# Optimization experiments

Measured on AMD Instinct MI355X. Metric: run time of the kernel, lower is better.

Reference implementation:

```python
import jax, jax.numpy as jnp
import numpy as np

NEG_INF = -jnp.inf


def setup_inputs() -> dict:
    B, V = 128, 128000
    key = jax.random.key(0)
    k1, k2, k3, k4, k5 = jax.random.split(key, 5)
    logits = jax.random.normal(k1, (B, V), dtype=jnp.float32)
    # temperatures in [0.1, 1.0) to avoid divide-by-tiny blowups
    temperatures = jax.random.uniform(k2, (B,), dtype=jnp.float32) * 0.9 + 0.1
    # min_p typically small, in [0, 0.1)
    min_ps = jax.random.uniform(k3, (B,), dtype=jnp.float32) * 0.1
    # top_p in [0.1, 1.0)
    top_ps = jax.random.uniform(k4, (B,), dtype=jnp.float32) * 0.9 + 0.1
    # top_k in [1, 1000)
    top_ks = jax.random.randint(k5, (B,), 1, 1000, dtype=jnp.int32)
    return {"logits": logits, "temperatures": temperatures, "min_ps": min_ps,
            "top_ps": top_ps, "top_ks": top_ks}


def _apply_top_k_top_p(logits, top_ps, top_ks):
    B, V = logits.shape
    sort_idx = jnp.argsort(logits, axis=-1)  # ascending, matches torch sort(descending=False)
    logits_sort = jnp.take_along_axis(logits, sort_idx, axis=-1)
    # top-k: threshold is the (V-k)-th smallest value; mask anything strictly below it
    thresh_idx = (V - top_ks.astype(jnp.int32))[:, None]          # [B,1]
    thresh = jnp.take_along_axis(logits_sort, thresh_idx, axis=-1)  # [B,1]
    logits_sort = jnp.where(logits_sort < thresh, NEG_INF, logits_sort)
    # top-p: drop smallest tokens whose cumulative prob <= 1 - p; never drop the max token
    probs_sort = jax.nn.softmax(logits_sort, axis=-1)
    probs_sum = jnp.cumsum(probs_sort, axis=-1)
    top_p_mask = probs_sum <= (1.0 - top_ps)[:, None]
    top_p_mask = top_p_mask.at[:, -1].set(False)
    logits_sort = jnp.where(top_p_mask, NEG_INF, logits_sort)
    # scatter back to original vocab order
    rows = jnp.arange(B)[:, None]
    return jnp.zeros_like(logits_sort).at[rows, sort_idx].set(logits_sort)


def _apply_min_p(logits, min_ps):
    probs = jax.nn.softmax(logits, axis=-1)
    top_probs = jnp.max(probs, axis=-1, keepdims=True)
    remove = probs < min_ps[:, None] * top_probs
    return jnp.where(remove, NEG_INF, logits)


def reference(logits, temperatures, min_ps, top_ps, top_ks):
    logits = logits.astype(jnp.float32) / temperatures[:, None]
    logits = _apply_top_k_top_p(logits, top_ps, top_ks)
    logits = _apply_min_p(logits, min_ps)
    # torch.multinomial(softmax(logits), 1) == categorical sampling from logits
    sample_key = jax.random.key(42)
    next_tokens = jax.random.categorical(sample_key, logits, axis=-1)  # [B]
    return next_tokens
```

## Files before the change

kernel.cpp:

```cpp
#include <hip/hip_runtime.h>
#include <stdint.h>

#define HBINS 4096
#define CAND 4096
#define SCAP 2048
#define CSLICES 16
#define CTHREADS 256
#define STHREADS 1024
#define TLOC 128
#define STAGECAP 1024

typedef unsigned int u32;
typedef unsigned long long u64;

__device__ __forceinline__ u32 f2s(float f) {
  u32 b = __float_as_uint(f);
  return b ^ ((b & 0x80000000u) ? 0xFFFFFFFFu : 0x80000000u);
}
__device__ __forceinline__ float s2f(u32 s) {
  u32 b = (s & 0x80000000u) ? (s ^ 0x80000000u) : ~s;
  return __uint_as_float(b);
}
__device__ __forceinline__ u32 rotl32(u32 x, int r) { return (x << r) | (x >> (32 - r)); }

__device__ __forceinline__ u64 shfl_xor_u64(u64 v, int mask) {
  int lo = __shfl_xor((int)(u32)v, mask, 64);
  int hi = __shfl_xor((int)(u32)(v >> 32), mask, 64);
  return ((u64)(u32)hi << 32) | (u32)lo;
}

__device__ __forceinline__ u32 threefry_bits(u32 ctr) {
  const u32 ks0 = 0u, ks1 = 42u, ks2 = 0x1BD11BDAu ^ 0u ^ 42u;
  u32 x0 = ks0;
  u32 x1 = ctr + ks1;
#define TFR(r) { x0 += x1; x1 = rotl32(x1, (r)); x1 ^= x0; }
  TFR(13) TFR(15) TFR(26) TFR(6)   x0 += ks1; x1 += ks2 + 1u;
  TFR(17) TFR(29) TFR(16) TFR(24)  x0 += ks2; x1 += ks0 + 2u;
  TFR(13) TFR(15) TFR(26) TFR(6)   x0 += ks0; x1 += ks1 + 3u;
  TFR(17) TFR(29) TFR(16) TFR(24)  x0 += ks1; x1 += ks2 + 4u;
  TFR(13) TFR(15) TFR(26) TFR(6)   x0 += ks2; x1 += ks0 + 5u;
#undef TFR
  return x0 ^ x1;
}

__global__ __launch_bounds__(CTHREADS)
void collect2_kernel(const float* __restrict__ logits,
                     const float* __restrict__ temps,
                     u32* __restrict__ gcount,
                     u64* __restrict__ gcand, int V, int slice_len) {
  const int row = blockIdx.x / CSLICES;
  const int sl  = blockIdx.x % CSLICES;
  const int tid = threadIdx.x;

  __shared__ u32 hist[HBINS];
  __shared__ u64 stage[STAGECAP];
  __shared__ u32 part[CTHREADS];
  __shared__ u32 chunkv[64];
  __shared__ int sh_thr, sh_cnt, sh_base;

  for (int i = tid; i < HBINS; i += CTHREADS) hist[i] = 0u;
  __syncthreads();

  int rem = V - sl * slice_len;
  if (rem > slice_len) rem = slice_len;
  if (rem < 0) rem = 0;
  const float* src = logits + (size_t)row * (size_t)V + (size_t)sl * slice_len;
  const int n4 = rem >> 2;
  const float4* p4 = (const float4*)src;

  for (int i = tid; i < n4; i += CTHREADS) {
    float4 w = p4[i];
    atomicAdd(&hist[f2s(w.x) >> 20], 1u);
    atomicAdd(&hist[f2s(w.y) >> 20], 1u);
    atomicAdd(&hist[f2s(w.z) >> 20], 1u);
    atomicAdd(&hist[f2s(w.w) >> 20], 1u);
  }
  for (int i = (n4 << 2) + tid; i < rem; i += CTHREADS)
    atomicAdd(&hist[f2s(src[i]) >> 20], 1u);
  __syncthreads();

  {
    u32 s = 0;
    for (int j = 0; j < 16; ++j) s += hist[tid * 16 + j];
    part[tid] = s;
  }
  __syncthreads();
  if (tid < 64)
    chunkv[tid] = part[tid * 4] + part[tid * 4 + 1] + part[tid * 4 + 2] + part[tid * 4 + 3];
  __syncthreads();
  if (tid == 0) {
    u32 ku = (u32)((rem < TLOC) ? (rem > 0 ? rem : 1) : TLOC);
    u32 acc = 0;
    int cstar = 0;
    for (int c = 63; c >= 0; --c) {
      if (acc + chunkv[c] >= ku) { cstar = c; break; }
      acc += chunkv[c];
    }
    int pstar = cstar * 4;
    for (int p = cstar * 4 + 3; p >= cstar * 4; --p) {
      if (acc + part[p] >= ku) { pstar = p; break; }
      acc += part[p];
    }
    int bstar = pstar * 16;
    for (int bq = pstar * 16 + 15; bq >= pstar * 16; --bq) {
      acc += hist[bq];
      if (acc >= ku) { bstar = bq; break; }
    }
    sh_thr = (int)(((u32)bstar) << 20);
    sh_cnt = 0;
  }
  __syncthreads();

  const u32 thr = (u32)sh_thr;
  const float t = temps[row];
  const u32 ibase = (u32)(sl * slice_len);
  for (int i = tid; i < n4; i += CTHREADS) {
    float4 w = p4[i];
    if (f2s(w.x) >= thr) { int pos = atomicAdd(&sh_cnt, 1); if (pos < STAGECAP) stage[pos] = ((u64)f2s(w.x / t) << 32) | (ibase + 4u * i + 0u); }
    if (f2s(w.y) >= thr) { int pos = atomicAdd(&sh_cnt, 1); if (pos < STAGECAP) stage[pos] = ((u64)f2s(w.y / t) << 32) | (ibase + 4u * i + 1u); }
    if (f2s(w.z) >= thr) { int pos = atomicAdd(&sh_cnt, 1); if (pos < STAGECAP) stage[pos] = ((u64)f2s(w.z / t) << 32) | (ibase + 4u * i + 2u); }
    if (f2s(w.w) >= thr) { int pos = atomicAdd(&sh_cnt, 1); if (pos < STAGECAP) stage[pos] = ((u64)f2s(w.w / t) << 32) | (ibase + 4u * i + 3u); }
  }
  for (int i = (n4 << 2) + tid; i < rem; i += CTHREADS) {
    float lg = src[i];
    if (f2s(lg) >= thr) { int pos = atomicAdd(&sh_cnt, 1); if (pos < STAGECAP) stage[pos] = ((u64)f2s(lg / t) << 32) | (ibase + (u32)i); }
  }
  __syncthreads();
  int n = sh_cnt;
  if (n > STAGECAP) n = STAGECAP;
  if (tid == 0) sh_base = (int)atomicAdd(&gcount[row], (u32)n);
  __syncthreads();
  const int base = sh_base;
  u64* gc = gcand + (size_t)row * CAND;
  for (int i = tid; i < n; i += CTHREADS) {
    int dst = base + i;
    if (dst < CAND) gc[dst] = stage[i];
  }
}

__global__ __launch_bounds__(STHREADS)
void Sampler_73529840107542_kernel(const float* __restrict__ minps,
                                   const float* __restrict__ topps,
                                   const int* __restrict__ topks,
                                   const u32* __restrict__ gcount,
                                   const u64* __restrict__ gcand,
                                   int* __restrict__ out, int V) {
  const int b = blockIdx.x;
  const int tid = threadIdx.x;
  const int w = tid >> 6, l = tid & 63;
  const float one_minus_p = 1.0f - topps[b];
  const float minp = minps[b];
  int k = topks[b];
  if (k < 1) k = 1;
  if (k > V) k = V;

  __shared__ __align__(16) unsigned char arena[50176];
  u64* cand   = (u64*)(arena);
  float* eBuf = (float*)(arena);
  unsigned char* keepf = arena + 8192;
  u64* scand  = (u64*)(arena + 32768);
  u32* rbin   = (u32*)(arena + 49152);
  __shared__ float wredf[16];
  __shared__ u64 wred64[16];
  __shared__ int sh_byte, sh_above, sh_ns;
  __shared__ float sh_Z1, sh_Z2;

  int cs = (int)gcount[b];
  if (cs > CAND) cs = CAND;
  const u64* gc = gcand + (size_t)b * CAND;
  for (int c = tid; c < cs; c += STHREADS) cand[c] = gc[c];
  if (tid == 0) sh_ns = 0;
  __syncthreads();

  u32 prefix = 0u;
  u32 remk = (u32)k;
  for (int pass = 0; pass < 4; ++pass) {
    const int shift = 24 - 8 * pass;
    if (tid < 256) rbin[tid] = 0u;
    __syncthreads();
    const u32 mask = (pass == 0) ? 0u : (0xFFFFFFFFu << (shift + 8));
    const int iters = (cs + STHREADS - 1) / STHREADS;
    for (int it = 0; it < iters; ++it) {
      int c = it * STHREADS + tid;
      bool active = false;
      u32 bin = 0;
      if (c < cs) {
        u32 s = (u32)(cand[c] >> 32);
        if (((s ^ prefix) & mask) == 0u) { active = true; bin = (s >> shift) & 255u; }
      }
      u64 ball = __ballot(active);
      while (ball) {
        int leader = __ffsll((unsigned long long)ball) - 1;
        u32 lbin = (u32)__shfl((int)bin, leader, 64);
        u64 same = __ballot(active && bin == lbin);
        if (l == leader) atomicAdd(&rbin[lbin], (u32)__popcll(same));
        ball &= ~same;
      }
    }
    __syncthreads();
    if (w == 0) {
      u32 b0 = rbin[4 * l], b1 = rbin[4 * l + 1], b2 = rbin[4 * l + 2], b3 = rbin[4 * l + 3];
      u32 q3 = b3, q2 = b2 + q3, q1 = b1 + q2, q0 = b0 + q1;
      u32 inc = q0;
#pragma unroll
      for (int off = 1; off < 64; off <<= 1) {
        int src = l + off;
        u32 o = (u32)__shfl((int)inc, src < 64 ? src : l, 64);
        inc += (src < 64) ? o : 0u;
      }
      u32 excl = inc - q0;
      u64 ball = __ballot(excl + q0 >= remk);
      int lsel = 63 - __clzll(ball);
      if (l == lsel) {
        int i; u32 above;
        if      (excl + q3 >= remk) { i = 3; above = excl; }
        else if (excl + q2 >= remk) { i = 2; above = excl + q3; }
        else if (excl + q1 >= remk) { i = 1; above = excl + q2; }
        else                        { i = 0; above = excl + q1; }
        sh_byte = 4 * l + i;
        sh_above = (int)above;
      }
    }
    __syncthreads();
    prefix |= ((u32)sh_byte) << shift;
    remk -= (u32)sh_above;
  }
  const u32 Ts = prefix;

  for (int c = tid; c < cs; c += STHREADS) {
    u64 key = cand[c];
    if ((u32)(key >> 32) >= Ts) {
      int pos = atomicAdd(&sh_ns, 1);
      if (pos < SCAP) scand[pos] = key;
    }
  }
  __syncthreads();
  int ns = sh_ns;
  if (ns > SCAP) ns = SCAP;

  int SN = 128;
  while (SN < ns) SN <<= 1;
  const int NW = SN >> 7;
  const bool act = (w < NW);
  const int e_lo = (w << 7) + l;
  const int e_hi = e_lo + 64;
  const u64 SENT = 0xFFFFFFFFFFFFFFFFull;
  u64 k0 = (act && e_lo < ns) ? scand[e_lo] : SENT;
  u64 k1 = (act && e_hi < ns) ? scand[e_hi] : SENT;
  for (int size = 2; size <= SN; size <<= 1) {
    for (int s = size >> 1; s > 0; s >>= 1) {
      if (s >= 128) {
        if (act) { scand[e_lo] = k0; scand[e_hi] = k1; }
        __syncthreads();
        if (act) {
          u64 p0 = scand[e_lo ^ s], p1 = scand[e_hi ^ s];
          bool km0 = (((e_lo & s) == 0) == ((e_lo & size) == 0));
          if (km0 ? (p0 < k0) : (p0 > k0)) k0 = p0;
          bool km1 = (((e_hi & s) == 0) == ((e_hi & size) == 0));
          if (km1 ? (p1 < k1) : (p1 > k1)) k1 = p1;
        }
        __syncthreads();
      } else if (act) {
        if (s == 64) {
          bool asc = ((e_lo & size) == 0);
          if ((k0 > k1) == asc) { u64 t = k0; k0 = k1; k1 = t; }
        } else {
          u64 p0 = shfl_xor_u64(k0, s);
          u64 p1 = shfl_xor_u64(k1, s);
          bool km0 = (((l & s) == 0) == ((e_lo & size) == 0));
          if (km0 ? (p0 < k0) : (p0 > k0)) k0 = p0;
          bool km1 = (((l & s) == 0) == ((e_hi & size) == 0));
          if (km1 ? (p1 < k1) : (p1 > k1)) k1 = p1;
        }
      }
    }
  }
  if (act) { scand[e_lo] = k0; scand[e_hi] = k1; }
  __syncthreads();

  const float m = s2f((u32)(scand[ns - 1] >> 32));

  for (int c = tid; c < ns; c += STHREADS)
    eBuf[c] = expf(s2f((u32)(scand[c] >> 32)) - m);
  __syncthreads();

  {
    float local = 0.0f;
    for (int c = tid; c < ns; c += STHREADS) local += eBuf[c];
#pragma unroll
    for (int off = 1; off < 64; off <<= 1) local += __shfl_xor(local, off, 64);
    if (l == 0) wredf[w] = local;
    __syncthreads();
    if (w == 0) {
      float v = (l < 16) ? wredf[l] : 0.0f;
#pragma unroll
      for (int off = 1; off < 64; off <<= 1) v += __shfl_xor(v, off, 64);
      if (l == 0) sh_Z1 = v;
    }
    __syncthreads();
  }
  const float Z1 = sh_Z1;

  if (w == 0) {
    float carry = 0.0f;
    for (int base2 = 0; base2 < ns; base2 += 64) {
      int c = base2 + l;
      float v = (c < ns) ? (eBuf[c] / Z1) : 0.0f;
      float acc = carry;
#pragma unroll 16
      for (int j = 0; j < 64; ++j) {
        float t = __shfl(v, j, 64);
        acc += (l >= j) ? t : 0.0f;
      }
      if (c < ns)
        keepf[c] = (c == ns - 1 || acc > one_minus_p) ? 1 : 0;
      carry = __shfl(acc, 63, 64);
    }
  }
  __syncthreads();

  {
    float local = 0.0f;
    for (int c = tid; c < ns; c += STHREADS)
      if (keepf[c]) local += eBuf[c];
#pragma unroll
    for (int off = 1; off < 64; off <<= 1) local += __shfl_xor(local, off, 64);
    if (l == 0) wredf[w] = local;
    __syncthreads();
    if (w == 0) {
      float v = (l < 16) ? wredf[l] : 0.0f;
#pragma unroll
      for (int off = 1; off < 64; off <<= 1) v += __shfl_xor(v, off, 64);
      if (l == 0) sh_Z2 = v;
    }
    __syncthreads();
  }

  {
    const float Z2 = sh_Z2;
    const float rhs = minp * (1.0f / Z2);
    for (int c = tid; c < ns; c += STHREADS)
      if (keepf[c] && (eBuf[c] / Z2 < rhs)) keepf[c] = 0;
  }
  __syncthreads();

  {
    const float TINY = 1.17549435082228750797e-38f;
    u64 best = 0ull;
    for (int c = tid; c < ns; c += STHREADS) {
      if (!keepf[c]) continue;
      u32 s = (u32)(scand[c] >> 32);
      u32 idx = (u32)(scand[c] & 0xFFFFFFFFull);
      float x = s2f(s);
      u32 bits = threefry_bits((u32)b * (u32)V + idx);
      float f = __uint_as_float((bits >> 9) | 0x3f800000u) - 1.0f;
      float u = fmaxf(TINY, f * 1.0f + TINY);
      float g = -logf(-logf(u));
      float sc = g + x;
      u64 key = ((u64)f2s(sc) << 32) | (u64)(0xFFFFFFFFu - idx);
      if (key > best) best = key;
    }
#pragma unroll
    for (int off = 1; off < 64; off <<= 1) {
      u64 o = shfl_xor_u64(best, off);
      if (o > best) best = o;
    }
    if (l == 0) wred64[w] = best;
    __syncthreads();
    if (w == 0) {
      u64 v = (l < 16) ? wred64[l] : 0ull;
#pragma unroll
      for (int off = 1; off < 64; off <<= 1) {
        u64 o = shfl_xor_u64(v, off);
        if (o > v) v = o;
      }
      if (l == 0) out[b] = (int)(0xFFFFFFFFu - (u32)(v & 0xFFFFFFFFull));
    }
  }
}

extern "C" void kernel_launch(void* const* d_in, const int* in_sizes, int n_in,
                              void* d_out, int out_size, void* d_ws, size_t ws_size,
                              hipStream_t stream) {
  const float* logits = (const float*)d_in[0];
  const float* temps  = (const float*)d_in[1];
  const float* minps  = (const float*)d_in[2];
  const float* topps  = (const float*)d_in[3];
  const int*   topks  = (const int*)d_in[4];
  const int B = in_sizes[1];
  const int V = in_sizes[0] / B;
  (void)n_in; (void)out_size; (void)ws_size;

  u32* gcount = (u32*)d_ws;
  u64* gcand  = (u64*)((char*)d_ws + ((B * 4 + 511) & ~511));

  const int slice_len = (((V + CSLICES - 1) / CSLICES) + 3) & ~3;

  hipMemsetAsync(gcount, 0, (size_t)B * sizeof(u32), stream);
  collect2_kernel<<<dim3(B * CSLICES), dim3(CTHREADS), 0, stream>>>(
      logits, temps, gcount, gcand, V, slice_len);
  Sampler_73529840107542_kernel<<<dim3(B), dim3(STHREADS), 0, stream>>>(
      minps, topps, topks, gcount, gcand, (int*)d_out, V);
}
```

Before: 180.3 us.

## Halve sampler block size, overlap top-p scan with Gumbel scoring

The second-stage sampler kernel drops from 1024 to 512 threads. The radix-select histogram now does plain atomics into four privatised bin copies instead of ballot-based aggregation. The top-p cumulative scan becomes a serial single-lane float4 loop that finds a cut index, while the other waves compute Gumbel scores for all candidates at the same time. The keep-flag passes are replaced by a cut index and a min-p check. A shared-memory bitonic fallback covers candidate counts above 1024, which trades some sort parallelism for fewer barriers and overlapped work.

After: 170.7 us. -5.3%, faster.

```diff
diff --git a/kernel.cpp b/kernel.cpp
--- a/kernel.cpp
+++ b/kernel.cpp
@@ -6,7 +6,7 @@
 #define SCAP 2048
 #define CSLICES 16
 #define CTHREADS 256
-#define STHREADS 1024
+#define STHREADS 512
 #define TLOC 128
 #define STAGECAP 1024
 
@@ -154,15 +154,16 @@
   if (k < 1) k = 1;
   if (k > V) k = V;
 
-  __shared__ __align__(16) unsigned char arena[50176];
+  __shared__ __align__(16) unsigned char arena[53248];
   u64* cand   = (u64*)(arena);
   float* eBuf = (float*)(arena);
-  unsigned char* keepf = arena + 8192;
+  float* pArr = (float*)(arena + 8192);
+  u64* gArr   = (u64*)(arena + 16384);
   u64* scand  = (u64*)(arena + 32768);
   u32* rbin   = (u32*)(arena + 49152);
-  __shared__ float wredf[16];
-  __shared__ u64 wred64[16];
-  __shared__ int sh_byte, sh_above, sh_ns;
+  __shared__ float wredf[8];
+  __shared__ u64 wred64[8];
+  __shared__ int sh_byte, sh_above, sh_ns, sh_ccut;
   __shared__ float sh_Z1, sh_Z2;
 
   int cs = (int)gcount[b];
@@ -174,32 +175,27 @@
 
   u32 prefix = 0u;
   u32 remk = (u32)k;
+  const int cp = (w & 3) << 8;
   for (int pass = 0; pass < 4; ++pass) {
     const int shift = 24 - 8 * pass;
-    if (tid < 256) rbin[tid] = 0u;
+    for (int i = tid; i < 1024; i += STHREADS) rbin[i] = 0u;
     __syncthreads();
     const u32 mask = (pass == 0) ? 0u : (0xFFFFFFFFu << (shift + 8));
-    const int iters = (cs + STHREADS - 1) / STHREADS;
-    for (int it = 0; it < iters; ++it) {
-      int c = it * STHREADS + tid;
-      bool active = false;
-      u32 bin = 0;
-      if (c < cs) {
-        u32 s = (u32)(cand[c] >> 32);
-        if (((s ^ prefix) & mask) == 0u) { active = true; bin = (s >> shift) & 255u; }
-      }
-      u64 ball = __ballot(active);
-      while (ball) {
-        int leader = __ffsll((unsigned long long)ball) - 1;
-        u32 lbin = (u32)__shfl((int)bin, leader, 64);
-        u64 same = __ballot(active && bin == lbin);
-        if (l == leader) atomicAdd(&rbin[lbin], (u32)__popcll(same));
-        ball &= ~same;
-      }
+    for (int c = tid; c < cs; c += STHREADS) {
+      u32 s = (u32)(cand[c] >> 32);
+      if (((s ^ prefix) & mask) == 0u)
+        atomicAdd(&rbin[cp + ((s >> shift) & 255u)], 1u);
     }
     __syncthreads();
     if (w == 0) {
-      u32 b0 = rbin[4 * l], b1 = rbin[4 * l + 1], b2 = rbin[4 * l + 2], b3 = rbin[4 * l + 3];
+      u32 b0 = 0, b1 = 0, b2 = 0, b3 = 0;
+#pragma unroll
+      for (int q = 0; q < 4; ++q) {
+        b0 += rbin[q * 256 + 4 * l];
+        b1 += rbin[q * 256 + 4 * l + 1];
+        b2 += rbin[q * 256 + 4 * l + 2];
+        b3 += rbin[q * 256 + 4 * l + 3];
+      }
       u32 q3 = b3, q2 = b2 + q3, q1 = b1 + q2, q0 = b0 + q1;
       u32 inc = q0;
 #pragma unroll
@@ -238,45 +234,65 @@
   int ns = sh_ns;
   if (ns > SCAP) ns = SCAP;
 
-  int SN = 128;
-  while (SN < ns) SN <<= 1;
-  const int NW = SN >> 7;
-  const bool act = (w < NW);
-  const int e_lo = (w << 7) + l;
-  const int e_hi = e_lo + 64;
   const u64 SENT = 0xFFFFFFFFFFFFFFFFull;
-  u64 k0 = (act && e_lo < ns) ? scand[e_lo] : SENT;
-  u64 k1 = (act && e_hi < ns) ? scand[e_hi] : SENT;
-  for (int size = 2; size <= SN; size <<= 1) {
-    for (int s = size >> 1; s > 0; s >>= 1) {
-      if (s >= 128) {
-        if (act) { scand[e_lo] = k0; scand[e_hi] = k1; }
-        __syncthreads();
-        if (act) {
-          u64 p0 = scand[e_lo ^ s], p1 = scand[e_hi ^ s];
-          bool km0 = (((e_lo & s) == 0) == ((e_lo & size) == 0));
-          if (km0 ? (p0 < k0) : (p0 > k0)) k0 = p0;
-          bool km1 = (((e_hi & s) == 0) == ((e_hi & size) == 0));
-          if (km1 ? (p1 < k1) : (p1 > k1)) k1 = p1;
+  if (ns <= 1024) {
+    int SN = 128;
+    while (SN < ns) SN <<= 1;
+    const int NW = SN >> 7;
+    const bool act = (w < NW);
+    const int e_lo = (w << 7) + l;
+    const int e_hi = e_lo + 64;
+    u64 k0 = (act && e_lo < ns) ? scand[e_lo] : SENT;
+    u64 k1 = (act && e_hi < ns) ? scand[e_hi] : SENT;
+    for (int size = 2; size <= SN; size <<= 1) {
+      for (int s = size >> 1; s > 0; s >>= 1) {
+        if (s >= 128) {
+          if (act) { scand[e_lo] = k0; scand[e_hi] = k1; }
+          __syncthreads();
+          if (act) {
+            u64 p0 = scand[e_lo ^ s], p1 = scand[e_hi ^ s];
+            bool km0 = (((e_lo & s) == 0) == ((e_lo & size) == 0));
+            if (km0 ? (p0 < k0) : (p0 > k0)) k0 = p0;
+            bool km1 = (((e_hi & s) == 0) == ((e_hi & size) == 0));
+            if (km1 ? (p1 < k1) : (p1 > k1)) k1 = p1;
+          }
+          __syncthreads();
+        } else if (act) {
+          if (s == 64) {
+            bool asc = ((e_lo & size) == 0);
+            if ((k0 > k1) == asc) { u64 t = k0; k0 = k1; k1 = t; }
+          } else {
+            u64 p0 = shfl_xor_u64(k0, s);
+            u64 p1 = shfl_xor_u64(k1, s);
+            bool km0 = (((l & s) == 0) == ((e_lo & size) == 0));
+            if (km0 ? (p0 < k0) : (p0 > k0)) k0 = p0;
+            bool km1 = (((l & s) == 0) == ((e_hi & size) == 0));
+            if (km1 ? (p1 < k1) : (p1 > k1)) k1 = p1;
+          }
+        }
+      }
+    }
+    if (act) { scand[e_lo] = k0; scand[e_hi] = k1; }
+    __syncthreads();
+  } else {
+    int SN = 128;
+    while (SN < ns) SN <<= 1;
+    for (int c = ns + tid; c < SN; c += STHREADS) scand[c] = SENT;
+    __syncthreads();
+    for (int size = 2; size <= SN; size <<= 1) {
+      for (int s = size >> 1; s > 0; s >>= 1) {
+        for (int i = tid; i < SN; i += STHREADS) {
+          int j = i ^ s;
+          if (j > i) {
+            u64 a = scand[i], b2 = scand[j];
+            bool asc = ((i & size) == 0);
+            if ((a > b2) == asc) { scand[i] = b2; scand[j] = a; }
+          }
         }
         __syncthreads();
-      } else if (act) {
-        if (s == 64) {
-          bool asc = ((e_lo & size) == 0);
-          if ((k0 > k1) == asc) { u64 t = k0; k0 = k1; k1 = t; }
-        } else {
-          u64 p0 = shfl_xor_u64(k0, s);
-          u64 p1 = shfl_xor_u64(k1, s);
-          bool km0 = (((l & s) == 0) == ((e_lo & size) == 0));
-          if (km0 ? (p0 < k0) : (p0 > k0)) k0 = p0;
-          bool km1 = (((l & s) == 0) == ((e_hi & size) == 0));
-          if (km1 ? (p1 < k1) : (p1 > k1)) k1 = p1;
-        }
-      }
-    }
-  }
-  if (act) { scand[e_lo] = k0; scand[e_hi] = k1; }
-  __syncthreads();
+      }
+    }
+  }
 
   const float m = s2f((u32)(scand[ns - 1] >> 32));
 
@@ -292,7 +308,7 @@
     if (l == 0) wredf[w] = local;
     __syncthreads();
     if (w == 0) {
-      float v = (l < 16) ? wredf[l] : 0.0f;
+      float v = (l < 8) ? wredf[l] : 0.0f;
 #pragma unroll
       for (int off = 1; off < 64; off <<= 1) v += __shfl_xor(v, off, 64);
       if (l == 0) sh_Z1 = v;
@@ -301,64 +317,71 @@
   }
   const float Z1 = sh_Z1;
 
+  const int nsp = (ns + 3) & ~3;
+  for (int c = tid; c < nsp; c += STHREADS)
+    pArr[c] = (c < ns) ? (eBuf[c] / Z1) : 0.0f;
+  __syncthreads();
+
   if (w == 0) {
-    float carry = 0.0f;
-    for (int base2 = 0; base2 < ns; base2 += 64) {
-      int c = base2 + l;
-      float v = (c < ns) ? (eBuf[c] / Z1) : 0.0f;
-      float acc = carry;
-#pragma unroll 16
-      for (int j = 0; j < 64; ++j) {
-        float t = __shfl(v, j, 64);
-        acc += (l >= j) ? t : 0.0f;
-      }
-      if (c < ns)
-        keepf[c] = (c == ns - 1 || acc > one_minus_p) ? 1 : 0;
-      carry = __shfl(acc, 63, 64);
-    }
-  }
-  __syncthreads();
-
-  {
-    float local = 0.0f;
-    for (int c = tid; c < ns; c += STHREADS)
-      if (keepf[c]) local += eBuf[c];
-#pragma unroll
-    for (int off = 1; off < 64; off <<= 1) local += __shfl_xor(local, off, 64);
-    if (l == 0) wredf[w] = local;
-    __syncthreads();
-    if (w == 0) {
-      float v = (l < 16) ? wredf[l] : 0.0f;
-#pragma unroll
-      for (int off = 1; off < 64; off <<= 1) v += __shfl_xor(v, off, 64);
-      if (l == 0) sh_Z2 = v;
-    }
-    __syncthreads();
-  }
-
-  {
-    const float Z2 = sh_Z2;
-    const float rhs = minp * (1.0f / Z2);
-    for (int c = tid; c < ns; c += STHREADS)
-      if (keepf[c] && (eBuf[c] / Z2 < rhs)) keepf[c] = 0;
-  }
-  __syncthreads();
-
-  {
+    if (l == 0) {
+      float acc = 0.0f;
+      int ccut = -1;
+      const float4* pq = (const float4*)pArr;
+      const int n4 = nsp >> 2;
+#pragma unroll 4
+      for (int i = 0; i < n4; ++i) {
+        float4 q = pq[i];
+        acc += q.x; if (ccut < 0 && acc > one_minus_p) ccut = 4 * i + 0;
+        acc += q.y; if (ccut < 0 && acc > one_minus_p) ccut = 4 * i + 1;
+        acc += q.z; if (ccut < 0 && acc > one_minus_p) ccut = 4 * i + 2;
+        acc += q.w; if (ccut < 0 && acc > one_minus_p) ccut = 4 * i + 3;
+      }
+      if (ccut < 0 || ccut > ns - 1) ccut = ns - 1;
+      sh_ccut = ccut;
+    }
+  } else {
     const float TINY = 1.17549435082228750797e-38f;
-    u64 best = 0ull;
-    for (int c = tid; c < ns; c += STHREADS) {
-      if (!keepf[c]) continue;
-      u32 s = (u32)(scand[c] >> 32);
-      u32 idx = (u32)(scand[c] & 0xFFFFFFFFull);
+    for (int c = (w - 1) * 64 + l; c < ns; c += (STHREADS - 64)) {
+      u64 key = scand[c];
+      u32 s = (u32)(key >> 32);
+      u32 idx = (u32)(key & 0xFFFFFFFFull);
       float x = s2f(s);
       u32 bits = threefry_bits((u32)b * (u32)V + idx);
       float f = __uint_as_float((bits >> 9) | 0x3f800000u) - 1.0f;
       float u = fmaxf(TINY, f * 1.0f + TINY);
       float g = -logf(-logf(u));
       float sc = g + x;
-      u64 key = ((u64)f2s(sc) << 32) | (u64)(0xFFFFFFFFu - idx);
-      if (key > best) best = key;
+      gArr[c] = ((u64)f2s(sc) << 32) | (u64)(0xFFFFFFFFu - idx);
+    }
+  }
+  __syncthreads();
+  const int ccut = sh_ccut;
+
+  {
+    float local = 0.0f;
+    for (int c = ccut + tid; c < ns; c += STHREADS) local += eBuf[c];
+#pragma unroll
+    for (int off = 1; off < 64; off <<= 1) local += __shfl_xor(local, off, 64);
+    if (l == 0) wredf[w] = local;
+    __syncthreads();
+    if (w == 0) {
+      float v = (l < 8) ? wredf[l] : 0.0f;
+#pragma unroll
+      for (int off = 1; off < 64; off <<= 1) v += __shfl_xor(v, off, 64);
+      if (l == 0) sh_Z2 = v;
+    }
+    __syncthreads();
+  }
+  const float Z2 = sh_Z2;
+
+  {
+    const float rhs = minp * (1.0f / Z2);
+    u64 best = 0ull;
+    for (int c = ccut + tid; c < ns; c += STHREADS) {
+      if (eBuf[c] / Z2 >= rhs) {
+        u64 o = gArr[c];
+        if (o > best) best = o;
+      }
     }
 #pragma unroll
     for (int off = 1; off < 64; off <<= 1) {
@@ -368,7 +391,7 @@
     if (l == 0) wred64[w] = best;
     __syncthreads();
     if (w == 0) {
-      u64 v = (l < 16) ? wred64[l] : 0ull;
+      u64 v = (l < 8) ? wred64[l] : 0ull;
 #pragma unroll
       for (int off = 1; off < 64; off <<= 1) {
         u64 o = shfl_xor_u64(v, off);
```
